# Kernel tuning notes

Hardware: AMD Instinct MI355X
Metric: run time of the kernel (lower is better)

Reference implementation:

```python
import jax, jax.numpy as jnp
import numpy as np

M = 8      # number of modalities (len(ModalityType))
D = 256    # embedding_dim
B = 8192   # batch size


def setup_inputs() -> dict:
    key = jax.random.key(0)
    ks = jax.random.split(key, 12)
    s = 1.0 / np.sqrt(D)
    x = jax.random.normal(ks[0], (M, B, D), dtype=jnp.float32)
    reasoning_query = jax.random.normal(ks[1], (B, D), dtype=jnp.float32)
    # Per ordered modality pair (src, tgt): seq_len=1 MHA reduces to out_proj(V_proj(tgt)).
    Wv = jax.random.normal(ks[2], (M, M, D, D), dtype=jnp.float32) * s
    bv = jnp.zeros((M, M, D), dtype=jnp.float32)
    Wo = jax.random.normal(ks[3], (M, M, D, D), dtype=jnp.float32) * s
    bo = jnp.zeros((M, M, D), dtype=jnp.float32)
    # Per-modality fusion MLP: Linear(2D->D), ReLU, Linear(D->D)  (dropout = eval/identity)
    W1 = jax.random.normal(ks[4], (M, D, 2 * D), dtype=jnp.float32) * s
    b1 = jnp.zeros((M, D), dtype=jnp.float32)
    W2 = jax.random.normal(ks[5], (M, D, D), dtype=jnp.float32) * s
    b2 = jnp.zeros((M, D), dtype=jnp.float32)
    # Attention controller: Linear(2D->D), ReLU, Linear(D->1), Sigmoid
    Wc1 = jax.random.normal(ks[6], (D, 2 * D), dtype=jnp.float32) * s
    bc1 = jnp.zeros((D,), dtype=jnp.float32)
    wc2 = jax.random.normal(ks[7], (D,), dtype=jnp.float32) * s
    bc2 = jnp.zeros((1,), dtype=jnp.float32)
    return dict(x=x, reasoning_query=reasoning_query, Wv=Wv, bv=bv, Wo=Wo, bo=bo,
                W1=W1, b1=b1, W2=W2, b2=b2, Wc1=Wc1, bc1=bc1, wc2=wc2, bc2=bc2)


def reference(x, reasoning_query, Wv, bv, Wo, bo, W1, b1, W2, b2, Wc1, bc1, wc2, bc2):
    m = x.shape[0]
    # Cross-modal attention with seq_len=1: softmax over one key == 1, so the
    # attended output is exactly out_proj(V_proj(tgt_embedding)) for every pair.
    h = jnp.einsum('tbd,sted->stbe', x, Wv) + bv[:, :, None, :]          # [M,M,B,D]
    ctx = jnp.einsum('stbe,stoe->stbo', h, Wo) + bo[:, :, None, :]       # [M,M,B,D]
    # Mean over the M-1 target modalities (src != tgt), matching stack(...).mean(-1)
    offdiag = (1.0 - jnp.eye(m, dtype=x.dtype))[:, :, None, None]
    cross = (ctx * offdiag).sum(axis=1) / (m - 1)                         # [M,B,D]
    # Per-modality fusion MLP on cat([original, cross])
    comb = jnp.concatenate([x, cross], axis=-1)                           # [M,B,2D]
    hid = jax.nn.relu(jnp.einsum('mbf,mdf->mbd', comb, W1) + b1[:, None, :])
    fused = jnp.einsum('mbd,mod->mbo', hid, W2) + b2[:, None, :]          # [M,B,D]
    # Reasoning-query gating controller
    q = jnp.broadcast_to(reasoning_query[None], fused.shape)              # [M,B,D]
    qc = jnp.concatenate([q, fused], axis=-1)                             # [M,B,2D]
    ch = jax.nn.relu(jnp.einsum('mbf,df->mbd', qc, Wc1) + bc1)
    score = jax.nn.sigmoid(jnp.einsum('mbd,d->mb', ch, wc2) + bc2)        # [M,B]
    gated = fused * score[..., None]
    unified = gated.mean(axis=0)                                          # [B,D]
    return unified
```

## Files before the change

kernel.cpp:

```cpp
#include <hip/hip_runtime.h>

#define MMOD 8
#define BB 8192
#define DD 256

typedef unsigned short u16;
typedef __attribute__((ext_vector_type(8))) short s16x8;
typedef __attribute__((ext_vector_type(4))) float f32x4;
typedef __attribute__((ext_vector_type(8))) unsigned short u16x8;

typedef __attribute__((address_space(3))) unsigned short lds_u16;
typedef __attribute__((address_space(1))) const unsigned short gl_u16;

__device__ __forceinline__ float b2f(u16 u){ union{unsigned i; float f;} x; x.i=((unsigned)u)<<16; return x.f; }
__device__ __forceinline__ u16 f2b(float f){ union{float f; unsigned i;} x; x.f=f; unsigned r = x.i + 0x7FFF + ((x.i>>16)&1u); return (u16)(r>>16); }

__device__ __forceinline__ void async_cp16(const u16* g, u16* l){
  __builtin_amdgcn_global_load_lds((gl_u16*)g, (lds_u16*)l, 16, 0, 0);
}

struct ConvArgs {
  const float* src[10];
  u16*         dst[10];
  int          n[10];
};
__global__ void convert_kernel(ConvArgs a){
  const long long stride = (long long)gridDim.x * blockDim.x;
  const long long base   = (long long)blockIdx.x * blockDim.x + threadIdx.x;
  for (int s = 0; s < 10; s++){
    const int n  = a.n[s];
    const int n8 = n >> 3;
    const float* sp = a.src[s];
    u16* dst = a.dst[s];
    for (long long i = base; i < n8; i += stride){
      float4 lo = ((const float4*)sp)[i*2];
      float4 hi = ((const float4*)sp)[i*2+1];
      u16x8 p;
      p[0]=f2b(lo.x); p[1]=f2b(lo.y); p[2]=f2b(lo.z); p[3]=f2b(lo.w);
      p[4]=f2b(hi.x); p[5]=f2b(hi.y); p[6]=f2b(hi.z); p[7]=f2b(hi.w);
      *(u16x8*)(dst + (i<<3)) = p;
    }
    for (long long i = ((long long)n8<<3) + base; i < n; i += stride)
      dst[i] = f2b(sp[i]);
  }
}

__device__ __forceinline__ s16x8 load8_f32(const float* p, long long idx){
  float4 lo = *(const float4*)(p + idx);
  float4 hi = *(const float4*)(p + idx + 4);
  s16x8 r;
  r[0]=(short)f2b(lo.x); r[1]=(short)f2b(lo.y); r[2]=(short)f2b(lo.z); r[3]=(short)f2b(lo.w);
  r[4]=(short)f2b(hi.x); r[5]=(short)f2b(hi.y); r[6]=(short)f2b(hi.z); r[7]=(short)f2b(hi.w);
  return r;
}

struct GArgs {
  const u16* A;  long long a_z; long long a_piece; int lda;
  const u16* A2; long long a2_z;
  const u16* B;  long long b_z; int ldb;
  u16*       C;  long long c_z; long long c_npiece; int ldc;
  const u16* bias; long long bias_z;
  const float* cbias;
  const u16* addm;
  const u16* wc2;
  float*     scores;
  float scale;
  int K;
  int relu;
};

__global__ __launch_bounds__(256, 2) void gemm_bt(GArgs g){
  alignas(16) __shared__ u16 lA[128*64];
  alignas(16) __shared__ u16 lB[128*64];
  const int tid  = threadIdx.x;
  const int lane = tid & 63;
  const int w    = tid >> 6;
  const int z    = blockIdx.z;

  const u16* Bbase = g.B + (long long)z * g.b_z + (long long)(blockIdx.y * 128) * g.ldb;

  f32x4 acc[4][4];
  #pragma unroll
  for (int i=0;i<4;i++)
    #pragma unroll
    for (int j=0;j<4;j++)
      #pragma unroll
      for (int r=0;r<4;r++) acc[i][j][r] = 0.0f;

  const int wr = (w >> 1) * 64, wc = (w & 1) * 64;
  const int fm = lane & 15;
  const int fk = (lane >> 4) * 8;
  const long long arow0 = (long long)blockIdx.x * 128;

  const int sr = lane >> 3;
  const int sq = (lane & 7) ^ sr;

  for (int k0 = 0; k0 < g.K; k0 += 64){
    const u16* Abase0 = (g.A2 && k0 >= 256) ? (g.A2 + (long long)z * g.a2_z)
                                            : (g.A  + (long long)z * g.a_z);
    const u16* At = Abase0 + (long long)(k0 >> 8) * g.a_piece + (k0 & 255);
    const u16* Bt = Bbase + k0;
    __syncthreads();
    #pragma unroll
    for (int i=0;i<4;i++){
      int r = i*32 + w*8 + sr;
      async_cp16(At + (arow0 + r) * (long long)g.lda + sq*8, lA + (i*256 + w*64) * 8);
      async_cp16(Bt + (long long)r * g.ldb + sq*8, lB + (i*256 + w*64) * 8);
    }
    __syncthreads();
    #pragma unroll
    for (int kk = 0; kk < 64; kk += 32){
      s16x8 af[4], bfr[4];
      const int qf = (kk + fk) >> 3;
      #pragma unroll
      for (int mi=0; mi<4; mi++){
        int r = wr + mi*16 + fm;
        af[mi] = *(const s16x8*)(lA + (r*8 + (qf ^ (r & 7))) * 8);
      }
      #pragma unroll
      for (int ni=0; ni<4; ni++){
        int r = wc + ni*16 + fm;
        bfr[ni] = *(const s16x8*)(lB + (r*8 + (qf ^ (r & 7))) * 8);
      }
      #pragma unroll
      for (int mi=0; mi<4; mi++)
        #pragma unroll
        for (int ni=0; ni<4; ni++)
          acc[mi][ni] = __builtin_amdgcn_mfma_f32_16x16x32_bf16(af[mi], bfr[ni], acc[mi][ni], 0, 0, 0);
    }
  }

  u16* Cb = g.C + (long long)z * g.c_z;
  const u16* biasp = g.bias ? g.bias + (long long)z * g.bias_z : (const u16*)0;
  #pragma unroll
  for (int mi=0; mi<4; mi++){
    #pragma unroll
    for (int ni=0; ni<4; ni++){
      int n = blockIdx.y*128 + wc + ni*16 + fm;
      float bb = 0.0f;
      if (g.cbias) bb = g.cbias[n];
      else if (biasp) bb = b2f(biasp[n]);
      long long cn = ((long long)(n >> 8)) * g.c_npiece + (n & 255);
      #pragma unroll
      for (int r=0; r<4; r++){
        long long b = arow0 + wr + mi*16 + (lane>>4)*4 + r;
        float v = acc[mi][ni][r] * g.scale + bb;
        if (g.addm) v += b2f(g.addm[b*256 + n]);
        if (g.relu) v = v > 0.0f ? v : 0.0f;
        Cb[cn + b * (long long)g.ldc] = f2b(v);
      }
    }
  }
}

__global__ __launch_bounds__(256, 4) void gemm_thin(GArgs g){
  alignas(16) __shared__ u16 lA[64*64];
  alignas(16) __shared__ u16 lB[256*64];
  const int tid  = threadIdx.x;
  const int lane = tid & 63;
  const int w    = tid >> 6;
  const int z    = blockIdx.z;

  const u16* Bbase = g.B + (long long)z * g.b_z;

  f32x4 acc[16];
  #pragma unroll
  for (int j=0;j<16;j++)
    #pragma unroll
    for (int r=0;r<4;r++) acc[j][r] = 0.0f;

  const int fm = lane & 15;
  const int fk = (lane >> 4) * 8;
  const long long arow0 = (long long)blockIdx.x * 64;

  const int sr = lane >> 3;
  const int sq = (lane & 7) ^ sr;

  for (int k0 = 0; k0 < g.K; k0 += 64){
    const u16* Abase0 = (g.A2 && k0 >= 256) ? (g.A2 + (long long)z * g.a2_z)
                                            : (g.A  + (long long)z * g.a_z);
    const u16* At = Abase0 + (long long)(k0 >> 8) * g.a_piece + (k0 & 255);
    const u16* Bt = Bbase + k0;
    __syncthreads();
    #pragma unroll
    for (int i=0;i<2;i++){
      int r = i*32 + w*8 + sr;
      async_cp16(At + (arow0 + r) * (long long)g.lda + sq*8, lA + (i*256 + w*64) * 8);
    }
    #pragma unroll
    for (int i=0;i<8;i++){
      int r = i*32 + w*8 + sr;
      async_cp16(Bt + (long long)r * g.ldb + sq*8, lB + (i*256 + w*64) * 8);
    }
    __syncthreads();
    #pragma unroll
    for (int kk = 0; kk < 64; kk += 32){
      const int qf = (kk + fk) >> 3;
      int ra = w*16 + fm;
      s16x8 af = *(const s16x8*)(lA + (ra*8 + (qf ^ (ra & 7))) * 8);
      #pragma unroll
      for (int ni=0; ni<16; ni++){
        int r = ni*16 + fm;
        s16x8 bfr = *(const s16x8*)(lB + (r*8 + (qf ^ (r & 7))) * 8);
        acc[ni] = __builtin_amdgcn_mfma_f32_16x16x32_bf16(af, bfr, acc[ni], 0, 0, 0);
      }
    }
  }

  u16* Cb = g.C + (long long)z * g.c_z;
  const u16* biasp = g.bias ? g.bias + (long long)z * g.bias_z : (const u16*)0;
  #pragma unroll
  for (int ni=0; ni<16; ni++){
    int n = ni*16 + fm;
    float bb = 0.0f;
    if (g.cbias) bb = g.cbias[n];
    else if (biasp) bb = b2f(biasp[n]);
    #pragma unroll
    for (int r=0; r<4; r++){
      long long b = arow0 + w*16 + (lane>>4)*4 + r;
      float v = acc[ni][r] * g.scale + bb;
      if (g.addm) v += b2f(g.addm[b*256 + n]);
      if (g.relu) v = v > 0.0f ? v : 0.0f;
      Cb[b * (long long)g.ldc + n] = f2b(v);
    }
  }
}

__global__ __launch_bounds__(256, 4) void gemm_score(GArgs g){
  alignas(16) __shared__ u16 lA[64*64];
  alignas(16) __shared__ u16 lB[256*64];
  const int tid  = threadIdx.x;
  const int lane = tid & 63;
  const int w    = tid >> 6;
  const int z    = blockIdx.z;

  const u16* Bbase = g.B;

  f32x4 acc[16];
  #pragma unroll
  for (int j=0;j<16;j++)
    #pragma unroll
    for (int r=0;r<4;r++) acc[j][r] = 0.0f;

  const int fm = lane & 15;
  const int fk = (lane >> 4) * 8;
  const long long arow0 = (long long)blockIdx.x * 64;

  const int sr = lane >> 3;
  const int sq = (lane & 7) ^ sr;

  for (int k0 = 0; k0 < g.K; k0 += 64){
    const u16* At = g.A + (long long)z * g.a_z + k0;
    const u16* Bt = Bbase + k0;
    __syncthreads();
    #pragma unroll
    for (int i=0;i<2;i++){
      int r = i*32 + w*8 + sr;
      async_cp16(At + (arow0 + r) * (long long)g.lda + sq*8, lA + (i*256 + w*64) * 8);
    }
    #pragma unroll
    for (int i=0;i<8;i++){
      int r = i*32 + w*8 + sr;
      async_cp16(Bt + (long long)r * g.ldb + sq*8, lB + (i*256 + w*64) * 8);
    }
    __syncthreads();
    #pragma unroll
    for (int kk = 0; kk < 64; kk += 32){
      const int qf = (kk + fk) >> 3;
      int ra = w*16 + fm;
      s16x8 af = *(const s16x8*)(lA + (ra*8 + (qf ^ (ra & 7))) * 8);
      #pragma unroll
      for (int ni=0; ni<16; ni++){
        int r = ni*16 + fm;
        s16x8 bfr = *(const s16x8*)(lB + (r*8 + (qf ^ (r & 7))) * 8);
        acc[ni] = __builtin_amdgcn_mfma_f32_16x16x32_bf16(af, bfr, acc[ni], 0, 0, 0);
      }
    }
  }

  float p[4] = {0.f, 0.f, 0.f, 0.f};
  #pragma unroll
  for (int ni=0; ni<16; ni++){
    int n = ni*16 + fm;
    float bb = b2f(g.bias[n]);
    float wcv = b2f(g.wc2[n]);
    #pragma unroll
    for (int r=0; r<4; r++){
      long long b = arow0 + w*16 + (lane>>4)*4 + r;
      float v = acc[ni][r] + bb + b2f(g.addm[b*256 + n]);
      v = v > 0.0f ? v : 0.0f;
      p[r] += v * wcv;
    }
  }
  #pragma unroll
  for (int r=0; r<4; r++){
    #pragma unroll
    for (int off=1; off<16; off<<=1) p[r] += __shfl_xor(p[r], off);
  }
  if (fm == 0){
    float bc2f = g.cbias[0];
    #pragma unroll
    for (int r=0; r<4; r++){
      long long b = arow0 + w*16 + (lane>>4)*4 + r;
      g.scores[(long long)z*BB + b] = 1.0f / (1.0f + __expf(-(p[r] + bc2f)));
    }
  }
}

__global__ __launch_bounds__(256, 2) void build_wb(const float* Wo, const float* Wv, u16* WB){
  alignas(16) __shared__ u16 lA[128*64];
  alignas(16) __shared__ u16 lB[128*64];
  const int tid  = threadIdx.x;
  const int lane = tid & 63;
  const int w    = tid >> 6;
  const int z = blockIdx.z, s = z >> 3, t = z & 7;
  const long long zoff = (long long)z * 65536;

  f32x4 acc[4][4];
  #pragma unroll
  for (int i=0;i<4;i++)
    #pragma unroll
    for (int j=0;j<4;j++)
      #pragma unroll
      for (int r=0;r<4;r++) acc[i][j][r] = 0.0f;

  const int wr = (w >> 1) * 64, wc = (w & 1) * 64;
  const int fm = lane & 15;
  const int fk = (lane >> 4) * 8;

  int srow[4], sq[4];
  #pragma unroll
  for (int i=0;i<4;i++){
    int c = i*256 + tid;
    srow[i] = c >> 3;
    sq[i]   = (c & 7) ^ (srow[i] & 7);
  }

  for (int k0 = 0; k0 < 256; k0 += 64){
    s16x8 va[4], vt[4];
    #pragma unroll
    for (int i=0;i<4;i++){
      long long aidx = zoff + (long long)(blockIdx.x*128 + srow[i]) * 256 + k0 + sq[i]*8;
      va[i] = load8_f32(Wo, aidx);
    }
    #pragma unroll
    for (int j=0;j<4;j++){
      int id = j*256 + tid;
      int e  = id >> 4;
      int dc = (id & 15) * 8;
      long long bidx = zoff + (long long)(k0 + e) * 256 + blockIdx.y*128 + dc;
      vt[j] = load8_f32(Wv, bidx);
    }
    __syncthreads();
    #pragma unroll
    for (int i=0;i<4;i++){
      int c = i*256 + tid;
      *(s16x8*)(lA + c*8) = va[i];
    }
    #pragma unroll
    for (int j=0;j<4;j++){
      int id = j*256 + tid;
      int e  = id >> 4;
      int dc = (id & 15) * 8;
      #pragma unroll
      for (int u=0; u<8; u++){
        int d = dc + u;
        lB[(d*8 + ((e>>3) ^ (d & 7)))*8 + (e & 7)] = (u16)vt[j][u];
      }
    }
    __syncthreads();
    #pragma unroll
    for (int kk = 0; kk < 64; kk += 32){
      s16x8 af[4], bfr[4];
      const int qf = (kk + fk) >> 3;
      #pragma unroll
      for (int mi=0; mi<4; mi++){
        int r = wr + mi*16 + fm;
        af[mi] = *(const s16x8*)(lA + (r*8 + (qf ^ (r & 7))) * 8);
      }
      #pragma unroll
      for (int ni=0; ni<4; ni++){
        int r = wc + ni*16 + fm;
        bfr[ni] = *(const s16x8*)(lB + (r*8 + (qf ^ (r & 7))) * 8);
      }
      #pragma unroll
      for (int mi=0; mi<4; mi++)
        #pragma unroll
        for (int ni=0; ni<4; ni++)
          acc[mi][ni] = __builtin_amdgcn_mfma_f32_16x16x32_bf16(af[mi], bfr[ni], acc[mi][ni], 0, 0, 0);
    }
    __syncthreads();
  }
  const int diag = (s == t);
  #pragma unroll
  for (int mi=0; mi<4; mi++){
    #pragma unroll
    for (int ni=0; ni<4; ni++){
      int d = blockIdx.y*128 + wc + ni*16 + fm;
      #pragma unroll
      for (int r=0; r<4; r++){
        int o = blockIdx.x*128 + wr + mi*16 + (lane>>4)*4 + r;
        float v = diag ? 0.0f : acc[mi][ni][r];
        WB[(long long)(s*256 + o) * 2048 + t*256 + d] = f2b(v);
      }
    }
  }
}

__global__ __launch_bounds__(256) void cb_kernel(const float* bv, const float* Wo, const float* bo, float* cb){
  int z = blockIdx.x, s = z >> 3, t = z & 7;
  if (s == t) return;
  int lane = threadIdx.x & 63, w = threadIdx.x >> 6;
  float4 bvv = *(const float4*)(bv + (long long)z*256 + lane*4);
  #pragma unroll
  for (int i=0; i<16; i++){
    int row = blockIdx.y*64 + w*16 + i;
    float4 wv4 = *(const float4*)(Wo + (long long)z*65536 + (long long)row*256 + lane*4);
    float p = wv4.x*bvv.x + wv4.y*bvv.y + wv4.z*bvv.z + wv4.w*bvv.w;
    #pragma unroll
    for (int off=32; off>0; off>>=1) p += __shfl_xor(p, off);
    if (lane == 0)
      atomicAdd(&cb[s*256 + row], (p + bo[(long long)z*256 + row]) * (1.0f/7.0f));
  }
}

__global__ __launch_bounds__(256) void final_gate(const u16* fused, const float* scores, float* out){
  int b = blockIdx.x;
  int tid = threadIdx.x;
  float sc[8];
  #pragma unroll
  for (int m=0; m<8; m++) sc[m] = scores[(long long)m*BB + b];
  float acc = 0.0f;
  #pragma unroll
  for (int m=0; m<8; m++)
    acc += b2f(fused[((long long)m*BB + b)*256 + tid]) * sc[m];
  out[(long long)b*256 + tid] = acc * 0.125f;
}

extern "C" void kernel_launch(void* const* d_in, const int* in_sizes, int n_in,
                              void* d_out, int out_size, void* d_ws, size_t ws_size,
                              hipStream_t stream){
  const float* x   = (const float*)d_in[0];
  const float* q   = (const float*)d_in[1];
  const float* Wv  = (const float*)d_in[2];
  const float* bv  = (const float*)d_in[3];
  const float* Wo  = (const float*)d_in[4];
  const float* bo  = (const float*)d_in[5];
  const float* W1  = (const float*)d_in[6];
  const float* b1  = (const float*)d_in[7];
  const float* W2  = (const float*)d_in[8];
  const float* b2  = (const float*)d_in[9];
  const float* Wc1 = (const float*)d_in[10];
  const float* bc1 = (const float*)d_in[11];
  const float* wc2 = (const float*)d_in[12];
  const float* bc2 = (const float*)d_in[13];

  char* ws = (char*)d_ws;
  u16*   xb    = (u16*)(ws + 0LL);
  u16*   qb    = (u16*)(ws + 33554432LL);
  u16*   cross = (u16*)(ws + 37748736LL);
  u16*   hid   = (u16*)(ws + 71303168LL);
  u16*   WB    = (u16*)(ws + 104857600LL);
  u16*   W1b   = (u16*)(ws + 113246208LL);
  u16*   W2b   = (u16*)(ws + 115343360LL);
  u16*   Wc1b  = (u16*)(ws + 116391936LL);
  u16*   b1b   = (u16*)(ws + 116654080LL);
  u16*   b2b   = (u16*)(ws + 116658176LL);
  u16*   bc1b  = (u16*)(ws + 116662272LL);
  u16*   wc2b  = (u16*)(ws + 116662784LL);
  float* bc2f  = (float*)(ws + 116663296LL);
  float* cb    = (float*)(ws + 116663424LL);
  u16*   fused = xb;
  u16*   qctx  = WB;
  float* scores = (float*)(ws + 104857600LL + 4194304LL);

  ConvArgs ca{};
  ca.src[0]=x;   ca.dst[0]=xb;   ca.n[0]=MMOD*BB*DD;
  ca.src[1]=q;   ca.dst[1]=qb;   ca.n[1]=BB*DD;
  ca.src[2]=W1;  ca.dst[2]=W1b;  ca.n[2]=MMOD*DD*2*DD;
  ca.src[3]=W2;  ca.dst[3]=W2b;  ca.n[3]=MMOD*DD*DD;
  ca.src[4]=Wc1; ca.dst[4]=Wc1b; ca.n[4]=DD*2*DD;
  ca.src[5]=b1;  ca.dst[5]=b1b;  ca.n[5]=MMOD*DD;
  ca.src[6]=b2;  ca.dst[6]=b2b;  ca.n[6]=MMOD*DD;
  ca.src[7]=bc1; ca.dst[7]=bc1b; ca.n[7]=DD;
  ca.src[8]=wc2; ca.dst[8]=wc2b; ca.n[8]=DD;
  ca.src[9]=bc2; ca.dst[9]=bc1b; ca.n[9]=0;
  convert_kernel<<<1024, 256, 0, stream>>>(ca);
  hipMemcpyAsync(bc2f, bc2, sizeof(float), hipMemcpyDeviceToDevice, stream);

  hipMemsetAsync(cb, 0, 2048*sizeof(float), stream);
  build_wb<<<dim3(2,2,64), 256, 0, stream>>>(Wo, Wv, WB);
  cb_kernel<<<dim3(64,4), 256, 0, stream>>>(bv, Wo, bo, cb);

  const long long BD = (long long)BB * DD;

  GArgs g2{};
  g2.A = xb; g2.a_z = 0; g2.a_piece = BD; g2.lda = 256; g2.A2 = 0; g2.a2_z = 0;
  g2.B = WB; g2.b_z = 0; g2.ldb = 2048;
  g2.C = cross; g2.c_z = 0; g2.c_npiece = BD; g2.ldc = 256;
  g2.bias = 0; g2.bias_z = 0; g2.cbias = cb; g2.addm = 0; g2.wc2 = 0; g2.scores = 0;
  g2.scale = 1.0f/7.0f; g2.K = 2048; g2.relu = 0;
  gemm_bt<<<dim3(64,16,1), 256, 0, stream>>>(g2);

  GArgs g5a{};
  g5a.A = qb; g5a.a_z = 0; g5a.a_piece = 0; g5a.lda = 256; g5a.A2 = 0; g5a.a2_z = 0;
  g5a.B = Wc1b; g5a.b_z = 0; g5a.ldb = 512;
  g5a.C = qctx; g5a.c_z = 0; g5a.c_npiece = 0; g5a.ldc = 256;
  g5a.bias = 0; g5a.bias_z = 0; g5a.cbias = 0; g5a.addm = 0; g5a.wc2 = 0; g5a.scores = 0;
  g5a.scale = 1.0f; g5a.K = 256; g5a.relu = 0;
  gemm_thin<<<dim3(128,1,1), 256, 0, stream>>>(g5a);

  GArgs g3{};
  g3.A = xb; g3.a_z = BD; g3.a_piece = 0; g3.lda = 256; g3.A2 = cross; g3.a2_z = BD;
  g3.B = W1b; g3.b_z = (long long)DD*2*DD; g3.ldb = 512;
  g3.C = hid; g3.c_z = BD; g3.c_npiece = 0; g3.ldc = 256;
  g3.bias = b1b; g3.bias_z = 256; g3.cbias = 0; g3.addm = 0; g3.wc2 = 0; g3.scores = 0;
  g3.scale = 1.0f; g3.K = 512; g3.relu = 1;
  gemm_thin<<<dim3(128,1,8), 256, 0, stream>>>(g3);

  GArgs g4{};
  g4.A = hid; g4.a_z = BD; g4.a_piece = 0; g4.lda = 256; g4.A2 = 0; g4.a2_z = 0;
  g4.B = W2b; g4.b_z = (long long)DD*DD; g4.ldb = 256;
  g4.C = fused; g4.c_z = BD; g4.c_npiece = 0; g4.ldc = 256;
  g4.bias = b2b; g4.bias_z = 256; g4.cbias = 0; g4.addm = 0; g4.wc2 = 0; g4.scores = 0;
  g4.scale = 1.0f; g4.K = 256; g4.relu = 0;
  gemm_thin<<<dim3(128,1,8), 256, 0, stream>>>(g4);

  GArgs g5b{};
  g5b.A = fused; g5b.a_z = BD; g5b.a_piece = 0; g5b.lda = 256; g5b.A2 = 0; g5b.a2_z = 0;
  g5b.B = Wc1b + 256; g5b.b_z = 0; g5b.ldb = 512;
  g5b.C = 0; g5b.c_z = 0; g5b.c_npiece = 0; g5b.ldc = 0;
  g5b.bias = bc1b; g5b.bias_z = 0; g5b.cbias = bc2f; g5b.addm = qctx;
  g5b.wc2 = wc2b; g5b.scores = scores;
  g5b.scale = 1.0f; g5b.K = 256; g5b.relu = 1;
  gemm_score<<<dim3(128,1,8), 256, 0, stream>>>(g5b);

  final_gate<<<dim3(BB), 256, 0, stream>>>(fused, scores, (float*)d_out);

  (void)in_sizes; (void)n_in; (void)out_size; (void)ws_size;
}
```

Measured before the change: 349.0 us.

## Fuse fusion MLP and gating controller GEMMs into one kernel with LDS-staged intermediates

Replaces the separate hidden-layer, output-layer, query-projection and score GEMM launches with a single per-modality kernel. The hidden activations and fused output stay in shared memory between stages, so the hid buffer and the qctx buffer are no longer written to and read back from global memory. The query projection is recomputed per modality inside the controller GEMM, which adds 8x redundant compute but removes a launch and a global add. The bias kernel now accumulates without atomics or a memset, and the bc2 copy is dropped. Larger LDS use lowers occupancy to 2 blocks per CU.

```diff
diff --git a/kernel.cpp b/kernel.cpp
--- a/kernel.cpp
+++ b/kernel.cpp
@@ -61,9 +61,6 @@
   u16*       C;  long long c_z; long long c_npiece; int ldc;
   const u16* bias; long long bias_z;
   const float* cbias;
-  const u16* addm;
-  const u16* wc2;
-  float*     scores;
   float scale;
   int K;
   int relu;
@@ -145,7 +142,6 @@
       for (int r=0; r<4; r++){
         long long b = arow0 + wr + mi*16 + (lane>>4)*4 + r;
         float v = acc[mi][ni][r] * g.scale + bb;
-        if (g.addm) v += b2f(g.addm[b*256 + n]);
         if (g.relu) v = v > 0.0f ? v : 0.0f;
         Cb[cn + b * (long long)g.ldc] = f2b(v);
       }
@@ -153,15 +149,27 @@
   }
 }
 
-__global__ __launch_bounds__(256, 4) void gemm_thin(GArgs g){
+struct MArgs {
+  const u16 *xb, *cross, *qb, *W1, *W2, *Wc1;
+  const u16 *b1, *b2, *bc1, *wc2;
+  const float* bc2;
+  u16* fused;
+  float* scores;
+};
+__global__ __launch_bounds__(256, 2) void gemm_mlp(MArgs g){
   alignas(16) __shared__ u16 lA[64*64];
   alignas(16) __shared__ u16 lB[256*64];
+  alignas(16) __shared__ u16 stage[4][64*64];
   const int tid  = threadIdx.x;
   const int lane = tid & 63;
   const int w    = tid >> 6;
-  const int z    = blockIdx.z;
-
-  const u16* Bbase = g.B + (long long)z * g.b_z;
+  const int m    = blockIdx.z;
+  const int fm   = lane & 15;
+  const int fk   = (lane >> 4) * 8;
+  const int sr   = lane >> 3;
+  const int sq   = (lane & 7) ^ sr;
+  const long long arow0 = (long long)blockIdx.x * 64;
+  const long long BD = (long long)BB * DD;
 
   f32x4 acc[16];
   #pragma unroll
@@ -169,34 +177,28 @@
     #pragma unroll
     for (int r=0;r<4;r++) acc[j][r] = 0.0f;
 
-  const int fm = lane & 15;
-  const int fk = (lane >> 4) * 8;
-  const long long arow0 = (long long)blockIdx.x * 64;
-
-  const int sr = lane >> 3;
-  const int sq = (lane & 7) ^ sr;
-
-  for (int k0 = 0; k0 < g.K; k0 += 64){
-    const u16* Abase0 = (g.A2 && k0 >= 256) ? (g.A2 + (long long)z * g.a2_z)
-                                            : (g.A  + (long long)z * g.a_z);
-    const u16* At = Abase0 + (long long)(k0 >> 8) * g.a_piece + (k0 & 255);
-    const u16* Bt = Bbase + k0;
+  const int ra = w*16 + fm;
+  const int myrow = w*16 + (lane>>4)*4;
+
+  for (int t = 0; t < 8; t++){
+    const int k0 = t*64;
+    const u16* At = (t < 4 ? g.xb : g.cross) + (long long)m * BD + (k0 & 255);
+    const u16* Bt = g.W1 + (long long)m * 131072 + k0;
     __syncthreads();
     #pragma unroll
     for (int i=0;i<2;i++){
       int r = i*32 + w*8 + sr;
-      async_cp16(At + (arow0 + r) * (long long)g.lda + sq*8, lA + (i*256 + w*64) * 8);
+      async_cp16(At + (arow0 + r) * 256LL + sq*8, lA + (i*256 + w*64) * 8);
     }
     #pragma unroll
     for (int i=0;i<8;i++){
       int r = i*32 + w*8 + sr;
-      async_cp16(Bt + (long long)r * g.ldb + sq*8, lB + (i*256 + w*64) * 8);
+      async_cp16(Bt + (long long)r * 512 + sq*8, lB + (i*256 + w*64) * 8);
     }
     __syncthreads();
     #pragma unroll
     for (int kk = 0; kk < 64; kk += 32){
       const int qf = (kk + fk) >> 3;
-      int ra = w*16 + fm;
       s16x8 af = *(const s16x8*)(lA + (ra*8 + (qf ^ (ra & 7))) * 8);
       #pragma unroll
       for (int ni=0; ni<16; ni++){
@@ -206,69 +208,39 @@
       }
     }
   }
-
-  u16* Cb = g.C + (long long)z * g.c_z;
-  const u16* biasp = g.bias ? g.bias + (long long)z * g.bias_z : (const u16*)0;
   #pragma unroll
   for (int ni=0; ni<16; ni++){
     int n = ni*16 + fm;
-    float bb = 0.0f;
-    if (g.cbias) bb = g.cbias[n];
-    else if (biasp) bb = b2f(biasp[n]);
+    float bb = b2f(g.b1[m*256 + n]);
+    int t = ni >> 2, k = n & 63, q = k >> 3, j = k & 7;
     #pragma unroll
     for (int r=0; r<4; r++){
-      long long b = arow0 + w*16 + (lane>>4)*4 + r;
-      float v = acc[ni][r] * g.scale + bb;
-      if (g.addm) v += b2f(g.addm[b*256 + n]);
-      if (g.relu) v = v > 0.0f ? v : 0.0f;
-      Cb[b * (long long)g.ldc + n] = f2b(v);
-    }
-  }
-}
-
-__global__ __launch_bounds__(256, 4) void gemm_score(GArgs g){
-  alignas(16) __shared__ u16 lA[64*64];
-  alignas(16) __shared__ u16 lB[256*64];
-  const int tid  = threadIdx.x;
-  const int lane = tid & 63;
-  const int w    = tid >> 6;
-  const int z    = blockIdx.z;
-
-  const u16* Bbase = g.B;
-
-  f32x4 acc[16];
+      int row = myrow + r;
+      float v = acc[ni][r] + bb;
+      v = v > 0.0f ? v : 0.0f;
+      stage[t][(row*8 + (q ^ (row & 7)))*8 + j] = f2b(v);
+    }
+  }
   #pragma unroll
   for (int j=0;j<16;j++)
     #pragma unroll
     for (int r=0;r<4;r++) acc[j][r] = 0.0f;
-
-  const int fm = lane & 15;
-  const int fk = (lane >> 4) * 8;
-  const long long arow0 = (long long)blockIdx.x * 64;
-
-  const int sr = lane >> 3;
-  const int sq = (lane & 7) ^ sr;
-
-  for (int k0 = 0; k0 < g.K; k0 += 64){
-    const u16* At = g.A + (long long)z * g.a_z + k0;
-    const u16* Bt = Bbase + k0;
-    __syncthreads();
-    #pragma unroll
-    for (int i=0;i<2;i++){
-      int r = i*32 + w*8 + sr;
-      async_cp16(At + (arow0 + r) * (long long)g.lda + sq*8, lA + (i*256 + w*64) * 8);
-    }
+  __syncthreads();
+
+  for (int t = 0; t < 4; t++){
+    const int k0 = t*64;
+    const u16* Bt = g.W2 + (long long)m * 65536 + k0;
+    __syncthreads();
     #pragma unroll
     for (int i=0;i<8;i++){
       int r = i*32 + w*8 + sr;
-      async_cp16(Bt + (long long)r * g.ldb + sq*8, lB + (i*256 + w*64) * 8);
+      async_cp16(Bt + (long long)r * 256 + sq*8, lB + (i*256 + w*64) * 8);
     }
     __syncthreads();
     #pragma unroll
     for (int kk = 0; kk < 64; kk += 32){
       const int qf = (kk + fk) >> 3;
-      int ra = w*16 + fm;
-      s16x8 af = *(const s16x8*)(lA + (ra*8 + (qf ^ (ra & 7))) * 8);
+      s16x8 af = *(const s16x8*)(&stage[t][(ra*8 + (qf ^ (ra & 7))) * 8]);
       #pragma unroll
       for (int ni=0; ni<16; ni++){
         int r = ni*16 + fm;
@@ -277,17 +249,75 @@
       }
     }
   }
-
-  float p[4] = {0.f, 0.f, 0.f, 0.f};
+  u16 fv[16][4];
   #pragma unroll
   for (int ni=0; ni<16; ni++){
     int n = ni*16 + fm;
-    float bb = b2f(g.bias[n]);
+    float bb = b2f(g.b2[m*256 + n]);
+    #pragma unroll
+    for (int r=0; r<4; r++){
+      long long b = arow0 + myrow + r;
+      u16 h = f2b(acc[ni][r] + bb);
+      fv[ni][r] = h;
+      g.fused[(long long)m * BD + b*256 + n] = h;
+    }
+  }
+  __syncthreads();
+  #pragma unroll
+  for (int ni=0; ni<16; ni++){
+    int n = ni*16 + fm;
+    int t = ni >> 2, k = n & 63, q = k >> 3, j = k & 7;
+    #pragma unroll
+    for (int r=0; r<4; r++){
+      int row = myrow + r;
+      stage[t][(row*8 + (q ^ (row & 7)))*8 + j] = fv[ni][r];
+    }
+  }
+  #pragma unroll
+  for (int j=0;j<16;j++)
+    #pragma unroll
+    for (int r=0;r<4;r++) acc[j][r] = 0.0f;
+  __syncthreads();
+
+  for (int t = 0; t < 8; t++){
+    const int k0 = t*64;
+    const u16* Bt = g.Wc1 + k0;
+    __syncthreads();
+    if (t < 4){
+      #pragma unroll
+      for (int i=0;i<2;i++){
+        int r = i*32 + w*8 + sr;
+        async_cp16(g.qb + (arow0 + r) * 256LL + k0 + sq*8, lA + (i*256 + w*64) * 8);
+      }
+    }
+    #pragma unroll
+    for (int i=0;i<8;i++){
+      int r = i*32 + w*8 + sr;
+      async_cp16(Bt + (long long)r * 512 + sq*8, lB + (i*256 + w*64) * 8);
+    }
+    __syncthreads();
+    #pragma unroll
+    for (int kk = 0; kk < 64; kk += 32){
+      const int qf = (kk + fk) >> 3;
+      s16x8 af = (t < 4) ? *(const s16x8*)(lA + (ra*8 + (qf ^ (ra & 7))) * 8)
+                         : *(const s16x8*)(&stage[t-4][(ra*8 + (qf ^ (ra & 7))) * 8]);
+      #pragma unroll
+      for (int ni=0; ni<16; ni++){
+        int r = ni*16 + fm;
+        s16x8 bfr = *(const s16x8*)(lB + (r*8 + (qf ^ (r & 7))) * 8);
+        acc[ni] = __builtin_amdgcn_mfma_f32_16x16x32_bf16(af, bfr, acc[ni], 0, 0, 0);
+      }
+    }
+  }
+  float p[4] = {0.f, 0.f, 0.f, 0.f};
+  #pragma unroll
+  for (int ni=0; ni<16; ni++){
+    int n = ni*16 + fm;
+    float bb = b2f(g.bc1[n]);
     float wcv = b2f(g.wc2[n]);
     #pragma unroll
     for (int r=0; r<4; r++){
-      long long b = arow0 + w*16 + (lane>>4)*4 + r;
-      float v = acc[ni][r] + bb + b2f(g.addm[b*256 + n]);
+      float v = acc[ni][r] + bb;
       v = v > 0.0f ? v : 0.0f;
       p[r] += v * wcv;
     }
@@ -298,11 +328,11 @@
     for (int off=1; off<16; off<<=1) p[r] += __shfl_xor(p[r], off);
   }
   if (fm == 0){
-    float bc2f = g.cbias[0];
+    float bc2v = g.bc2[0];
     #pragma unroll
     for (int r=0; r<4; r++){
-      long long b = arow0 + w*16 + (lane>>4)*4 + r;
-      g.scores[(long long)z*BB + b] = 1.0f / (1.0f + __expf(-(p[r] + bc2f)));
+      long long b = arow0 + myrow + r;
+      g.scores[(long long)m*BB + b] = 1.0f / (1.0f + __expf(-(p[r] + bc2v)));
     }
   }
 }
@@ -408,19 +438,29 @@
 }
 
 __global__ __launch_bounds__(256) void cb_kernel(const float* bv, const float* Wo, const float* bo, float* cb){
-  int z = blockIdx.x, s = z >> 3, t = z & 7;
-  if (s == t) return;
+  int s = blockIdx.x;
   int lane = threadIdx.x & 63, w = threadIdx.x >> 6;
-  float4 bvv = *(const float4*)(bv + (long long)z*256 + lane*4);
   #pragma unroll
   for (int i=0; i<16; i++){
     int row = blockIdx.y*64 + w*16 + i;
-    float4 wv4 = *(const float4*)(Wo + (long long)z*65536 + (long long)row*256 + lane*4);
-    float p = wv4.x*bvv.x + wv4.y*bvv.y + wv4.z*bvv.z + wv4.w*bvv.w;
-    #pragma unroll
-    for (int off=32; off>0; off>>=1) p += __shfl_xor(p, off);
-    if (lane == 0)
-      atomicAdd(&cb[s*256 + row], (p + bo[(long long)z*256 + row]) * (1.0f/7.0f));
+    float accv = 0.0f;
+    for (int t=0; t<8; t++){
+      if (t == s) continue;
+      int z = s*8 + t;
+      float4 bvv = *(const float4*)(bv + (long long)z*256 + lane*4);
+      float4 wv4 = *(const float4*)(Wo + (long long)z*65536 + (long long)row*256 + lane*4);
+      accv += wv4.x*bvv.x + wv4.y*bvv.y + wv4.z*bvv.z + wv4.w*bvv.w;
+    }
+    #pragma unroll
+    for (int off=32; off>0; off>>=1) accv += __shfl_xor(accv, off);
+    if (lane == 0){
+      float bsum = 0.0f;
+      for (int t=0; t<8; t++){
+        if (t == s) continue;
+        bsum += bo[(long long)(s*8+t)*256 + row];
+      }
+      cb[s*256 + row] = (accv + bsum) * (1.0f/7.0f);
+    }
   }
 }
 
@@ -459,7 +499,7 @@
   u16*   xb    = (u16*)(ws + 0LL);
   u16*   qb    = (u16*)(ws + 33554432LL);
   u16*   cross = (u16*)(ws + 37748736LL);
-  u16*   hid   = (u16*)(ws + 71303168LL);
+  u16*   fused = (u16*)(ws + 71303168LL);
   u16*   WB    = (u16*)(ws + 104857600LL);
   u16*   W1b   = (u16*)(ws + 113246208LL);
   u16*   W2b   = (u16*)(ws + 115343360LL);
@@ -468,11 +508,8 @@
   u16*   b2b   = (u16*)(ws + 116658176LL);
   u16*   bc1b  = (u16*)(ws + 116662272LL);
   u16*   wc2b  = (u16*)(ws + 116662784LL);
-  float* bc2f  = (float*)(ws + 116663296LL);
-  float* cb    = (float*)(ws + 116663424LL);
-  u16*   fused = xb;
-  u16*   qctx  = WB;
-  float* scores = (float*)(ws + 104857600LL + 4194304LL);
+  float* scores= (float*)(ws + 116663424LL);
+  float* cb    = (float*)(ws + 116925568LL);
 
   ConvArgs ca{};
   ca.src[0]=x;   ca.dst[0]=xb;   ca.n[0]=MMOD*BB*DD;
@@ -484,13 +521,11 @@
   ca.src[6]=b2;  ca.dst[6]=b2b;  ca.n[6]=MMOD*DD;
   ca.src[7]=bc1; ca.dst[7]=bc1b; ca.n[7]=DD;
   ca.src[8]=wc2; ca.dst[8]=wc2b; ca.n[8]=DD;
-  ca.src[9]=bc2; ca.dst[9]=bc1b; ca.n[9]=0;
+  ca.src[9]=wc2; ca.dst[9]=wc2b; ca.n[9]=0;
   convert_kernel<<<1024, 256, 0, stream>>>(ca);
-  hipMemcpyAsync(bc2f, bc2, sizeof(float), hipMemcpyDeviceToDevice, stream);
-
-  hipMemsetAsync(cb, 0, 2048*sizeof(float), stream);
+
   build_wb<<<dim3(2,2,64), 256, 0, stream>>>(Wo, Wv, WB);
-  cb_kernel<<<dim3(64,4), 256, 0, stream>>>(bv, Wo, bo, cb);
+  cb_kernel<<<dim3(8,4), 256, 0, stream>>>(bv, Wo, bo, cb);
 
   const long long BD = (long long)BB * DD;
 
@@ -498,42 +533,17 @@
   g2.A = xb; g2.a_z = 0; g2.a_piece = BD; g2.lda = 256; g2.A2 = 0; g2.a2_z = 0;
   g2.B = WB; g2.b_z = 0; g2.ldb = 2048;
   g2.C = cross; g2.c_z = 0; g2.c_npiece = BD; g2.ldc = 256;
-  g2.bias = 0; g2.bias_z = 0; g2.cbias = cb; g2.addm = 0; g2.wc2 = 0; g2.scores = 0;
+  g2.bias = 0; g2.bias_z = 0; g2.cbias = cb;
   g2.scale = 1.0f/7.0f; g2.K = 2048; g2.relu = 0;
   gemm_bt<<<dim3(64,16,1), 256, 0, stream>>>(g2);
 
-  GArgs g5a{};
-  g5a.A = qb; g5a.a_z = 0; g5a.a_piece = 0; g5a.lda = 256; g5a.A2 = 0; g5a.a2_z = 0;
-  g5a.B = Wc1b; g5a.b_z = 0; g5a.ldb = 512;
-  g5a.C = qctx; g5a.c_z = 0; g5a.c_npiece = 0; g5a.ldc = 256;
-  g5a.bias = 0; g5a.bias_z = 0; g5a.cbias = 0; g5a.addm = 0; g5a.wc2 = 0; g5a.scores = 0;
-  g5a.scale = 1.0f; g5a.K = 256; g5a.relu = 0;
-  gemm_thin<<<dim3(128,1,1), 256, 0, stream>>>(g5a);
-
-  GArgs g3{};
-  g3.A = xb; g3.a_z = BD; g3.a_piece = 0; g3.lda = 256; g3.A2 = cross; g3.a2_z = BD;
-  g3.B = W1b; g3.b_z = (long long)DD*2*DD; g3.ldb = 512;
-  g3.C = hid; g3.c_z = BD; g3.c_npiece = 0; g3.ldc = 256;
-  g3.bias = b1b; g3.bias_z = 256; g3.cbias = 0; g3.addm = 0; g3.wc2 = 0; g3.scores = 0;
-  g3.scale = 1.0f; g3.K = 512; g3.relu = 1;
-  gemm_thin<<<dim3(128,1,8), 256, 0, stream>>>(g3);
-
-  GArgs g4{};
-  g4.A = hid; g4.a_z = BD; g4.a_piece = 0; g4.lda = 256; g4.A2 = 0; g4.a2_z = 0;
-  g4.B = W2b; g4.b_z = (long long)DD*DD; g4.ldb = 256;
-  g4.C = fused; g4.c_z = BD; g4.c_npiece = 0; g4.ldc = 256;
-  g4.bias = b2b; g4.bias_z = 256; g4.cbias = 0; g4.addm = 0; g4.wc2 = 0; g4.scores = 0;
-  g4.scale = 1.0f; g4.K = 256; g4.relu = 0;
-  gemm_thin<<<dim3(128,1,8), 256, 0, stream>>>(g4);
-
-  GArgs g5b{};
-  g5b.A = fused; g5b.a_z = BD; g5b.a_piece = 0; g5b.lda = 256; g5b.A2 = 0; g5b.a2_z = 0;
-  g5b.B = Wc1b + 256; g5b.b_z = 0; g5b.ldb = 512;
-  g5b.C = 0; g5b.c_z = 0; g5b.c_npiece = 0; g5b.ldc = 0;
-  g5b.bias = bc1b; g5b.bias_z = 0; g5b.cbias = bc2f; g5b.addm = qctx;
-  g5b.wc2 = wc2b; g5b.scores = scores;
-  g5b.scale = 1.0f; g5b.K = 256; g5b.relu = 1;
-  gemm_score<<<dim3(128,1,8), 256, 0, stream>>>(g5b);
+  MArgs gm{};
+  gm.xb = xb; gm.cross = cross; gm.qb = qb;
+  gm.W1 = W1b; gm.W2 = W2b; gm.Wc1 = Wc1b;
+  gm.b1 = b1b; gm.b2 = b2b; gm.bc1 = bc1b; gm.wc2 = wc2b;
+  gm.bc2 = bc2;
+  gm.fused = fused; gm.scores = scores;
+  gemm_mlp<<<dim3(128,1,8), 256, 0, stream>>>(gm);
 
   final_gate<<<dim3(BB), 256, 0, stream>>>(fused, scores, (float*)d_out);
 
```

Measured after the change: 376.4 us. 1.08x slower.
